# Kernel tuning notes

Hardware: AMD Instinct MI355X
Metric: run time of the kernel (lower is better)

## Reference

```python
import jax, jax.numpy as jnp
import numpy as np

B, C, H, W = 4, 256, 64, 64
DQK = C // 4


def setup_inputs() -> dict:
    key = jax.random.key(0)
    ks = jax.random.split(key, 5)
    s = 0.05
    x = jax.random.normal(ks[0], (B, C, H, W), dtype=jnp.float32)
    Wq = jax.random.normal(ks[1], (DQK, C), dtype=jnp.float32) * s
    Wk = jax.random.normal(ks[2], (DQK, C), dtype=jnp.float32) * s
    Wv = jax.random.normal(ks[3], (C, C), dtype=jnp.float32) * s
    bq = jnp.zeros((DQK,), jnp.float32)
    bk = jnp.zeros((DQK,), jnp.float32)
    bv = jnp.zeros((C,), jnp.float32)
    gamma = jnp.zeros((1,), jnp.float32)
    return {"x": x, "Wq": Wq, "bq": bq, "Wk": Wk, "bk": bk,
            "Wv": Wv, "bv": bv, "gamma": gamma}


def reference(x, Wq, bq, Wk, bk, Wv, bv, gamma):
    b, c, h, w = x.shape
    n = h * w
    xf = x.reshape(b, c, n)                      # [B, C, N]
    # 1x1 convs == per-pixel linear projections
    q = jnp.einsum('dc,bcn->bnd', Wq, xf) + bq   # [B, N, Dqk]
    k = jnp.einsum('dc,bcn->bdn', Wk, xf) + bk[None, :, None]  # [B, Dqk, N]
    v = jnp.einsum('ec,bcn->ben', Wv, xf) + bv[None, :, None]  # [B, C, N]
    energy = jnp.einsum('bnd,bdm->bnm', q, k)    # [B, N, N]
    attn = jax.nn.softmax(energy, axis=-1)       # softmax over keys
    # out[b,c,i] = sum_j v[b,c,j] * attn[b,i,j]
    out = jnp.einsum('bcj,bij->bci', v, attn)    # [B, C, N]
    out = out.reshape(b, c, h, w)
    return gamma * out + x
```

## Files before the change

### kernel.cpp

```cpp
#include <hip/hip_runtime.h>

#define B_ 4
#define C_ 256
#define N_ 4096
#define D_ 64

typedef __bf16 bf16x8 __attribute__((ext_vector_type(8)));
typedef float floatx4 __attribute__((ext_vector_type(4)));
typedef unsigned short ushort8v __attribute__((ext_vector_type(8)));
typedef unsigned short ushort4v __attribute__((ext_vector_type(4)));

static __device__ __forceinline__ unsigned short f2bf(float f) {
    unsigned int u = __builtin_bit_cast(unsigned int, f);
    u += 0x7fffu + ((u >> 16) & 1u);
    return (unsigned short)(u >> 16);
}
static __device__ __forceinline__ float bf2f(unsigned short h) {
    unsigned int u = ((unsigned int)h) << 16;
    return __builtin_bit_cast(float, u);
}

#define GLOAD16(gp, lp)                                                      \
    __builtin_amdgcn_global_load_lds(                                        \
        (const __attribute__((address_space(1))) void*)(gp),                 \
        (__attribute__((address_space(3))) void*)(lp), 16, 0, 0)

__global__ __launch_bounds__(256, 3) void proj_kernel(
    const float* __restrict__ x,
    const float* __restrict__ Wq, const float* __restrict__ bq,
    const float* __restrict__ Wk, const float* __restrict__ bk,
    const float* __restrict__ Wv, const float* __restrict__ bv,
    unsigned short* __restrict__ Qg, unsigned short* __restrict__ Kg,
    unsigned short* __restrict__ Vg)
{
    __shared__ __align__(16) unsigned short smem[64 * 264];
    unsigned short* xb = smem;
    unsigned short* Lt = smem;

    const int n0 = blockIdx.x * 64;
    const int f0 = blockIdx.y * 128;
    const int b  = blockIdx.z;
    const int t  = threadIdx.x;
    const int w  = t >> 6;
    const int lane = t & 63;
    const int g  = lane >> 4;
    const int m  = lane & 15;

#pragma unroll
    for (int k = 0; k < 16; ++k) {
        int e  = t + 256 * k;
        int c  = e >> 4;
        int n4 = (e & 15) * 4;
        float4 v = *(const float4*)(x + ((size_t)b*C_ + c)*N_ + n0 + n4);
        float vv[4] = {v.x, v.y, v.z, v.w};
#pragma unroll
        for (int j = 0; j < 4; ++j) {
            int n = n4 + j;
            xb[n*264 + (((c >> 3) ^ (n & 7)) << 3) + (c & 7)] = f2bf(vv[j]);
        }
    }

    float bias_[2][4];
    const float* wbase[2];
#pragma unroll
    for (int mt = 0; mt < 2; ++mt) {
#pragma unroll
        for (int r = 0; r < 4; ++r) {
            int fg = f0 + 32*w + 16*mt + 4*g + r;
            bias_[mt][r] = (fg < 64) ? bq[fg]
                         : (fg < 128) ? bk[fg - 64] : bv[fg - 128];
        }
        int f = f0 + 32*w + 16*mt + m;
        wbase[mt] = (f < 64)  ? (Wq + (size_t)f * C_)
                  : (f < 128) ? (Wk + (size_t)(f - 64) * C_)
                              : (Wv + (size_t)(f - 128) * C_);
    }

    floatx4 acc[2][4];
#pragma unroll
    for (int mt = 0; mt < 2; ++mt)
#pragma unroll
        for (int nt = 0; nt < 4; ++nt) acc[mt][nt] = (floatx4){0.f,0.f,0.f,0.f};

    __syncthreads();

#pragma unroll
    for (int ks = 0; ks < 8; ++ks) {
        bf16x8 af[2];
#pragma unroll
        for (int mt = 0; mt < 2; ++mt) {
            float4 wa = *(const float4*)(wbase[mt] + 32*ks + 8*g);
            float4 wb = *(const float4*)(wbase[mt] + 32*ks + 8*g + 4);
            ushort8v u;
            u[0]=f2bf(wa.x); u[1]=f2bf(wa.y); u[2]=f2bf(wa.z); u[3]=f2bf(wa.w);
            u[4]=f2bf(wb.x); u[5]=f2bf(wb.y); u[6]=f2bf(wb.z); u[7]=f2bf(wb.w);
            af[mt] = __builtin_bit_cast(bf16x8, u);
        }
#pragma unroll
        for (int nt = 0; nt < 4; ++nt) {
            int n = 16*nt + m;
            bf16x8 bfr = *(const bf16x8*)
                &xb[n*264 + (((4*ks + g) ^ (n & 7)) << 3)];
#pragma unroll
            for (int mt = 0; mt < 2; ++mt)
                acc[mt][nt] = __builtin_amdgcn_mfma_f32_16x16x32_bf16(
                                  af[mt], bfr, acc[mt][nt], 0, 0, 0);
        }
    }

    __syncthreads();

#pragma unroll
    for (int mt = 0; mt < 2; ++mt)
#pragma unroll
        for (int nt = 0; nt < 4; ++nt)
#pragma unroll
            for (int r = 0; r < 4; ++r)
                Lt[(32*w + 16*mt + 4*g + r)*72 + 16*nt + m] =
                    f2bf(acc[mt][nt][r] + bias_[mt][r]);
    __syncthreads();

    if (f0 == 0) {
#pragma unroll
        for (int k = 0; k < 4; ++k) {
            int e   = t + 256 * k;
            int fq0 = (e >> 6) * 8;
            int nl  = e & 63;
            ushort8v u;
#pragma unroll
            for (int j = 0; j < 8; ++j) u[j] = Lt[(fq0 + j)*72 + nl];
            unsigned short* dst = (fq0 < 64)
                ? (Qg + ((size_t)b*N_ + n0 + nl)*D_ + fq0)
                : (Kg + ((size_t)b*N_ + n0 + nl)*D_ + (fq0 - 64));
            *(ushort8v*)dst = u;
        }
    } else {
        const int cb = f0 - 128;
#pragma unroll
        for (int k = 0; k < 4; ++k) {
            int e  = t + 256 * k;
            int fr = e >> 3;
            int n8 = (e & 7) * 8;
            ushort8v u = *(const ushort8v*)&Lt[fr*72 + n8];
            *(ushort8v*)(Vg + ((size_t)b*C_ + cb + fr)*N_ + n0 + n8) = u;
        }
    }
}

__global__ __launch_bounds__(256, 2) void flash_kernel(
    const unsigned short* __restrict__ Qg, const unsigned short* __restrict__ Kg,
    const unsigned short* __restrict__ Vg,
    unsigned short* __restrict__ Opart, float* __restrict__ ML)
{
    __shared__ __align__(16) unsigned short Vlds[32 * 512];
    __shared__ __align__(16) unsigned short Klds[2][8 * 512];
    __shared__ __align__(16) unsigned short PA[8 * 64 * 8];
    __shared__ float AL[64];

    const int g8   = blockIdx.x;
    const int tile = blockIdx.y;
    const int half = g8 & 1;
    const int b    = g8 >> 1;
    const int n0   = tile * 64;
    const int t    = threadIdx.x;
    const int w    = t >> 6;
    const int lane = t & 63;
    const int g    = lane >> 4;
    const int m    = lane & 15;

    const unsigned short* Qb = Qg + ((size_t)b*N_ + n0)*D_;
    const unsigned short* Kb = Kg + (size_t)b*N_*D_;
    const unsigned short* Vb = Vg + (size_t)b*C_*N_;

    const int cstart = half * 32;
    const int cend   = cstart + 32;

    bf16x8 qf[2];
#pragma unroll
    for (int ks = 0; ks < 2; ++ks)
        qf[ks] = *(const bf16x8*)(Qb + (size_t)(16*w + m)*D_ + 32*ks + 8*g);

    floatx4 accO[4][4];
#pragma unroll
    for (int rt = 0; rt < 4; ++rt)
#pragma unroll
        for (int ct = 0; ct < 4; ++ct)
            accO[rt][ct] = (floatx4){0.f, 0.f, 0.f, 0.f};

    float mrow = -1e30f, lrow = 0.f;

#pragma unroll
    for (int u = 0; u < 2; ++u) {
        const unsigned short* gp =
            Kb + (size_t)(cstart*64 + 16*w + m)*D_ + 32*u + 8*g;
        GLOAD16(gp, &Klds[0][(2*w + u) * 512]);
    }
    __syncthreads();

    for (int t64 = cstart; t64 < cend; ++t64) {
        const int j0 = t64 * 64;
        const int kb = (t64 - cstart) & 1;

#pragma unroll
        for (int u = 0; u < 8; ++u) {
            int sidx = 8*w + u;
            int ks   = sidx >> 4;
            int cb   = sidx & 15;
            const unsigned short* gp =
                Vb + (size_t)(16*cb + m)*N_ + j0 + 32*ks + 8*g;
            GLOAD16(gp, &Vlds[sidx * 512]);
        }
        if (t64 + 1 < cend) {
#pragma unroll
            for (int u = 0; u < 2; ++u) {
                const unsigned short* gp =
                    Kb + (size_t)((t64+1)*64 + 16*w + m)*D_ + 32*u + 8*g;
                GLOAD16(gp, &Klds[kb ^ 1][(2*w + u) * 512]);
            }
        }

        floatx4 accST[4];
#pragma unroll
        for (int jt = 0; jt < 4; ++jt) accST[jt] = (floatx4){0.f, 0.f, 0.f, 0.f};
#pragma unroll
        for (int ks = 0; ks < 2; ++ks)
#pragma unroll
            for (int jt = 0; jt < 4; ++jt) {
                bf16x8 kfr = *(const bf16x8*)
                    &Klds[kb][(jt*2 + ks)*512 + lane*8];
                accST[jt] = __builtin_amdgcn_mfma_f32_16x16x32_bf16(
                                kfr, qf[ks], accST[jt], 0, 0, 0);
            }

        float mx = -1e30f;
#pragma unroll
        for (int jt = 0; jt < 4; ++jt)
#pragma unroll
            for (int r = 0; r < 4; ++r) mx = fmaxf(mx, accST[jt][r]);
        mx = fmaxf(mx, __shfl_xor(mx, 16));
        mx = fmaxf(mx, __shfl_xor(mx, 32));
        float mnew  = fmaxf(mrow, mx);
        float alpha = __expf(mrow - mnew);
        mrow = mnew;
        float p[4][4];
        float rs = 0.f;
#pragma unroll
        for (int jt = 0; jt < 4; ++jt)
#pragma unroll
            for (int r = 0; r < 4; ++r) {
                float e = __expf(accST[jt][r] - mnew);
                p[jt][r] = e;
                rs += e;
            }
        rs += __shfl_xor(rs, 16);
        rs += __shfl_xor(rs, 32);
        lrow = lrow * alpha + rs;

        if (g == 0) AL[16*w + m] = alpha;

#pragma unroll
        for (int jt = 0; jt < 4; ++jt) {
            ushort4v u;
#pragma unroll
            for (int r = 0; r < 4; ++r) u[r] = f2bf(p[jt][r]);
            int frag = (w*2 + (jt >> 1))*64 + 16*(2*(jt & 1) + (g >> 1)) + m;
            *(ushort4v*)&PA[frag*8 + 4*(g & 1)] = u;
        }

        __syncthreads();

#pragma unroll
        for (int rt = 0; rt < 4; ++rt) {
            floatx4 a4 = *(const floatx4*)&AL[16*rt + 4*g];
#pragma unroll
            for (int ct = 0; ct < 4; ++ct)
                accO[rt][ct] *= a4;
        }
#pragma unroll
        for (int ks = 0; ks < 2; ++ks) {
            bf16x8 pf[4];
#pragma unroll
            for (int rt = 0; rt < 4; ++rt)
                pf[rt] = *(const bf16x8*)&PA[((rt*2 + ks)*64 + lane)*8];
#pragma unroll
            for (int ct = 0; ct < 4; ++ct) {
                int sidx = ks*16 + 4*w + ct;
                bf16x8 vfrag = *(const bf16x8*)&Vlds[sidx*512 + lane*8];
#pragma unroll
                for (int rt = 0; rt < 4; ++rt)
                    accO[rt][ct] = __builtin_amdgcn_mfma_f32_16x16x32_bf16(
                                       pf[rt], vfrag, accO[rt][ct], 0, 0, 0);
            }
        }

        __syncthreads();
    }

    const size_t tbase = ((size_t)(half*B_ + b)*64 + tile);
    unsigned short* Ob = Opart + tbase * (C_ * 64);
    float* ml = ML + tbase * 128;

    if (g == 0) {
        ml[16*w + m]      = mrow;
        ml[64 + 16*w + m] = lrow;
    }

#pragma unroll
    for (int rt = 0; rt < 4; ++rt)
#pragma unroll
        for (int ct = 0; ct < 4; ++ct) {
            int c = 64*w + 16*ct + m;
            ushort4v u4;
#pragma unroll
            for (int r = 0; r < 4; ++r) u4[r] = f2bf(accO[rt][ct][r]);
            *(ushort4v*)(Ob + (size_t)c*64 + 16*rt + 4*g) = u4;
        }
}

__global__ __launch_bounds__(256) void combine_kernel(
    const unsigned short* __restrict__ Opart, const float* __restrict__ ML,
    const float* __restrict__ x, const float* __restrict__ gamma,
    float* __restrict__ out)
{
    __shared__ float sc0[64], sc1[64];
    const int tile  = blockIdx.x;
    const int chalf = blockIdx.y;
    const int b     = blockIdx.z;
    const int n0    = tile * 64;
    const int t     = threadIdx.x;

    if (t < 64) {
        const float* ml0 = ML + ((size_t)(0*B_ + b)*64 + tile)*128;
        const float* ml1 = ML + ((size_t)(1*B_ + b)*64 + tile)*128;
        float m0 = ml0[t], l0 = ml0[64 + t];
        float m1 = ml1[t], l1 = ml1[64 + t];
        float M  = fmaxf(m0, m1);
        float f0 = __expf(m0 - M), f1 = __expf(m1 - M);
        float L  = f0*l0 + f1*l1;
        float gm = gamma[0];
        sc0[t] = gm * f0 / L;
        sc1[t] = gm * f1 / L;
    }
    __syncthreads();

    const int nq = t & 15;
    const int c0 = (t >> 4) + 16 * 8 * chalf / 8;
    const float* xb = x   + (size_t)b*C_*N_;
    float*       ob = out + (size_t)b*C_*N_;
    const unsigned short* O0 = Opart + ((size_t)(0*B_ + b)*64 + tile)*(C_*64);
    const unsigned short* O1 = Opart + ((size_t)(1*B_ + b)*64 + tile)*(C_*64);

    float s0[4], s1[4];
#pragma unroll
    for (int k = 0; k < 4; ++k) { s0[k] = sc0[4*nq + k]; s1[k] = sc1[4*nq + k]; }

#pragma unroll 4
    for (int i = 0; i < 8; ++i) {
        int c = 128*chalf + 16*i + (t >> 4);
        float4 x4 = *(const float4*)(xb + (size_t)c*N_ + n0 + 4*nq);
        ushort4v a4 = *(const ushort4v*)(O0 + (size_t)c*64 + 4*nq);
        ushort4v b4 = *(const ushort4v*)(O1 + (size_t)c*64 + 4*nq);
        float4 y;
        y.x = s0[0]*bf2f(a4[0]) + s1[0]*bf2f(b4[0]) + x4.x;
        y.y = s0[1]*bf2f(a4[1]) + s1[1]*bf2f(b4[1]) + x4.y;
        y.z = s0[2]*bf2f(a4[2]) + s1[2]*bf2f(b4[2]) + x4.z;
        y.w = s0[3]*bf2f(a4[3]) + s1[3]*bf2f(b4[3]) + x4.w;
        *(float4*)(ob + (size_t)c*N_ + n0 + 4*nq) = y;
    }
    (void)c0;
}

extern "C" void kernel_launch(void* const* d_in, const int* in_sizes, int n_in,
                              void* d_out, int out_size, void* d_ws, size_t ws_size,
                              hipStream_t stream) {
    const float* x     = (const float*)d_in[0];
    const float* Wq    = (const float*)d_in[1];
    const float* bq    = (const float*)d_in[2];
    const float* Wk    = (const float*)d_in[3];
    const float* bk    = (const float*)d_in[4];
    const float* Wv    = (const float*)d_in[5];
    const float* bv    = (const float*)d_in[6];
    const float* gamma = (const float*)d_in[7];
    float* out = (float*)d_out;

    unsigned short* Qg = (unsigned short*)d_ws;
    unsigned short* Kg = Qg + (size_t)B_*N_*D_;
    unsigned short* Vg = Kg + (size_t)B_*N_*D_;
    unsigned short* Op = Vg + (size_t)B_*C_*N_;
    float* ML = (float*)(Op + (size_t)2*B_*64*C_*64);

    proj_kernel<<<dim3(64, 3, 4), 256, 0, stream>>>(x, Wq, bq, Wk, bk, Wv, bv,
                                                    Qg, Kg, Vg);
    flash_kernel<<<dim3(8, 64), 256, 0, stream>>>(Qg, Kg, Vg, Op, ML);
    combine_kernel<<<dim3(64, 2, 4), 256, 0, stream>>>(Op, ML, x, gamma, out);
}
```

Baseline: 184.6 us.

## Fuse split-KV combine into flash kernel via last-arriver atomic ticket

```diff
diff --git a/kernel.cpp b/kernel.cpp
--- a/kernel.cpp
+++ b/kernel.cpp
@@ -31,10 +31,10 @@
     const float* __restrict__ Wk, const float* __restrict__ bk,
     const float* __restrict__ Wv, const float* __restrict__ bv,
     unsigned short* __restrict__ Qg, unsigned short* __restrict__ Kg,
-    unsigned short* __restrict__ Vg)
+    unsigned short* __restrict__ Vg, unsigned int* __restrict__ Tick)
 {
     __shared__ __align__(16) unsigned short smem[64 * 264];
-    unsigned short* xb = smem;
+    unsigned short* xs = smem;
     unsigned short* Lt = smem;
 
     const int n0 = blockIdx.x * 64;
@@ -46,6 +46,8 @@
     const int g  = lane >> 4;
     const int m  = lane & 15;
 
+    if (blockIdx.y == 0 && t == 0) Tick[b * 64 + blockIdx.x] = 0;
+
 #pragma unroll
     for (int k = 0; k < 16; ++k) {
         int e  = t + 256 * k;
@@ -56,7 +58,7 @@
 #pragma unroll
         for (int j = 0; j < 4; ++j) {
             int n = n4 + j;
-            xb[n*264 + (((c >> 3) ^ (n & 7)) << 3) + (c & 7)] = f2bf(vv[j]);
+            xs[n*264 + (((c >> 3) ^ (n & 7)) << 3) + (c & 7)] = f2bf(vv[j]);
         }
     }
 
@@ -100,7 +102,7 @@
         for (int nt = 0; nt < 4; ++nt) {
             int n = 16*nt + m;
             bf16x8 bfr = *(const bf16x8*)
-                &xb[n*264 + (((4*ks + g) ^ (n & 7)) << 3)];
+                &xs[n*264 + (((4*ks + g) ^ (n & 7)) << 3)];
 #pragma unroll
             for (int mt = 0; mt < 2; ++mt)
                 acc[mt][nt] = __builtin_amdgcn_mfma_f32_16x16x32_bf16(
@@ -150,12 +152,16 @@
 __global__ __launch_bounds__(256, 2) void flash_kernel(
     const unsigned short* __restrict__ Qg, const unsigned short* __restrict__ Kg,
     const unsigned short* __restrict__ Vg,
-    unsigned short* __restrict__ Opart, float* __restrict__ ML)
+    unsigned short* __restrict__ Op, float* __restrict__ ML,
+    unsigned int* __restrict__ Tick,
+    const float* __restrict__ x, const float* __restrict__ gamma,
+    float* __restrict__ out)
 {
     __shared__ __align__(16) unsigned short Vlds[32 * 512];
     __shared__ __align__(16) unsigned short Klds[2][8 * 512];
     __shared__ __align__(16) unsigned short PA[8 * 64 * 8];
     __shared__ float AL[64];
+    __shared__ int doneFlag;
 
     const int g8   = blockIdx.x;
     const int tile = blockIdx.y;
@@ -221,7 +227,7 @@
 
         floatx4 accST[4];
 #pragma unroll
-        for (int jt = 0; jt < 4; ++jt) accST[jt] = (floatx4){0.f, 0.f, 0.f, 0.f};
+        for (int jt = 0; jt < 4; ++jt) accST[jt] = (floatx4){0.f,0.f,0.f,0.f};
 #pragma unroll
         for (int ks = 0; ks < 2; ++ks)
 #pragma unroll
@@ -297,7 +303,7 @@
     }
 
     const size_t tbase = ((size_t)(half*B_ + b)*64 + tile);
-    unsigned short* Ob = Opart + tbase * (C_ * 64);
+    unsigned short* Ob = Op + tbase * (C_ * 64);
     float* ml = ML + tbase * 128;
 
     if (g == 0) {
@@ -315,20 +321,20 @@
             for (int r = 0; r < 4; ++r) u4[r] = f2bf(accO[rt][ct][r]);
             *(ushort4v*)(Ob + (size_t)c*64 + 16*rt + 4*g) = u4;
         }
-}
-
-__global__ __launch_bounds__(256) void combine_kernel(
-    const unsigned short* __restrict__ Opart, const float* __restrict__ ML,
-    const float* __restrict__ x, const float* __restrict__ gamma,
-    float* __restrict__ out)
-{
-    __shared__ float sc0[64], sc1[64];
-    const int tile  = blockIdx.x;
-    const int chalf = blockIdx.y;
-    const int b     = blockIdx.z;
-    const int n0    = tile * 64;
-    const int t     = threadIdx.x;
-
+
+    __threadfence();
+    __syncthreads();
+    if (t == 0) {
+        unsigned int old = atomicAdd(&Tick[b*64 + tile], 1u);
+        doneFlag = (old == 1);
+    }
+    __syncthreads();
+    if (!doneFlag) return;
+
+    __threadfence();
+
+    float* sc0 = (float*)Vlds;
+    float* sc1 = sc0 + 64;
     if (t < 64) {
         const float* ml0 = ML + ((size_t)(0*B_ + b)*64 + tile)*128;
         const float* ml1 = ML + ((size_t)(1*B_ + b)*64 + tile)*128;
@@ -344,19 +350,18 @@
     __syncthreads();
 
     const int nq = t & 15;
-    const int c0 = (t >> 4) + 16 * 8 * chalf / 8;
     const float* xb = x   + (size_t)b*C_*N_;
     float*       ob = out + (size_t)b*C_*N_;
-    const unsigned short* O0 = Opart + ((size_t)(0*B_ + b)*64 + tile)*(C_*64);
-    const unsigned short* O1 = Opart + ((size_t)(1*B_ + b)*64 + tile)*(C_*64);
+    const unsigned short* O0 = Op + ((size_t)(0*B_ + b)*64 + tile)*(C_*64);
+    const unsigned short* O1 = Op + ((size_t)(1*B_ + b)*64 + tile)*(C_*64);
 
     float s0[4], s1[4];
 #pragma unroll
     for (int k = 0; k < 4; ++k) { s0[k] = sc0[4*nq + k]; s1[k] = sc1[4*nq + k]; }
 
 #pragma unroll 4
-    for (int i = 0; i < 8; ++i) {
-        int c = 128*chalf + 16*i + (t >> 4);
+    for (int i = 0; i < 16; ++i) {
+        int c = 16*i + (t >> 4);
         float4 x4 = *(const float4*)(xb + (size_t)c*N_ + n0 + 4*nq);
         ushort4v a4 = *(const ushort4v*)(O0 + (size_t)c*64 + 4*nq);
         ushort4v b4 = *(const ushort4v*)(O1 + (size_t)c*64 + 4*nq);
@@ -367,7 +372,6 @@
         y.w = s0[3]*bf2f(a4[3]) + s1[3]*bf2f(b4[3]) + x4.w;
         *(float4*)(ob + (size_t)c*N_ + n0 + 4*nq) = y;
     }
-    (void)c0;
 }
 
 extern "C" void kernel_launch(void* const* d_in, const int* in_sizes, int n_in,
@@ -388,9 +392,10 @@
     unsigned short* Vg = Kg + (size_t)B_*N_*D_;
     unsigned short* Op = Vg + (size_t)B_*C_*N_;
     float* ML = (float*)(Op + (size_t)2*B_*64*C_*64);
+    unsigned int* Tick = (unsigned int*)(ML + (size_t)2*B_*64*128);
 
     proj_kernel<<<dim3(64, 3, 4), 256, 0, stream>>>(x, Wq, bq, Wk, bk, Wv, bv,
-                                                    Qg, Kg, Vg);
-    flash_kernel<<<dim3(8, 64), 256, 0, stream>>>(Qg, Kg, Vg, Op, ML);
-    combine_kernel<<<dim3(64, 2, 4), 256, 0, stream>>>(Op, ML, x, gamma, out);
+                                                    Qg, Kg, Vg, Tick);
+    flash_kernel<<<dim3(8, 64), 256, 0, stream>>>(Qg, Kg, Vg, Op, ML, Tick,
+                                                  x, gamma, out);
 }
```

Result: slower. 285.9 us (+54.9%).
